# Optimization experiments

Measured on AMD Instinct MI355X. Metric: run time of the kernel, lower is better.

Reference implementation:

```python
import jax, jax.numpy as jnp
import numpy as np

EPS = 1e-5

def bn(x, g, b, mu, var):
    # inference-mode BatchNorm2d (InPlaceABNSync, activation='none')
    scale = g * jax.lax.rsqrt(var + EPS)
    shift = b - mu * scale
    return x * scale[None, :, None, None] + shift[None, :, None, None]

def conv1x1(x, w):
    # w: [C_out, C_in]; x: [B, C_in, H, W]
    return jnp.einsum('oc,bchw->bohw', w, x)

def block(x, w1, g1, b1, m1, v1, w2, g2, b2, m2, v2):
    # conv1x1 -> BN -> ReLU -> conv1x1 -> BN -> ReLU
    h = jax.nn.relu(bn(conv1x1(x, w1), g1, b1, m1, v1))
    return jax.nn.relu(bn(conv1x1(h, w2), g2, b2, m2, v2))

def setup_inputs() -> dict:
    key = jax.random.key(0)
    ks = jax.random.split(key, 24)
    B, HID, H, W = 8, 10, 512, 512
    MID = 32
    d = {}
    d['xf']  = jax.random.normal(ks[0], (B, HID, H, W), jnp.float32)
    d['xh1'] = jax.random.normal(ks[1], (B, HID, H, W), jnp.float32)
    d['xh2'] = jax.random.normal(ks[2], (B, HID, H, W), jnp.float32)
    def mk_bn(k, c):
        k1, k2, k3, k4 = jax.random.split(k, 4)
        return (jax.random.normal(k1, (c,), jnp.float32) * 0.1 + 1.0,
                jax.random.normal(k2, (c,), jnp.float32) * 0.1,
                jax.random.normal(k3, (c,), jnp.float32) * 0.1,
                jnp.abs(jax.random.normal(k4, (c,), jnp.float32)) * 0.5 + 0.5)
    # conv_hf params
    d['w_hf1'] = jax.random.normal(ks[3], (MID, 2 * HID), jnp.float32) * (1.0 / np.sqrt(2 * HID))
    d['g_hf1'], d['b_hf1'], d['m_hf1'], d['v_hf1'] = mk_bn(ks[4], MID)
    d['w_hf2'] = jax.random.normal(ks[5], (HID, MID), jnp.float32) * (1.0 / np.sqrt(MID))
    d['g_hf2'], d['b_hf2'], d['m_hf2'], d['v_hf2'] = mk_bn(ks[6], HID)
    # conv_update params
    d['w_up1'] = jax.random.normal(ks[7], (MID, 2 * HID), jnp.float32) * (1.0 / np.sqrt(2 * HID))
    d['g_up1'], d['b_up1'], d['m_up1'], d['v_up1'] = mk_bn(ks[8], MID)
    d['w_up2'] = jax.random.normal(ks[9], (HID, MID), jnp.float32) * (1.0 / np.sqrt(MID))
    d['g_up2'], d['b_up2'], d['m_up2'], d['v_up2'] = mk_bn(ks[10], HID)
    return d

def reference(xf, xh1, xh2,
              w_hf1, g_hf1, b_hf1, m_hf1, v_hf1,
              w_hf2, g_hf2, b_hf2, m_hf2, v_hf2,
              w_up1, g_up1, b_up1, m_up1, v_up1,
              w_up2, g_up2, b_up2, m_up2, v_up2):
    message = block(jnp.concatenate([xh1, xh2], axis=1),
                    w_hf1, g_hf1, b_hf1, m_hf1, v_hf1,
                    w_hf2, g_hf2, b_hf2, m_hf2, v_hf2)
    xf_new = block(jnp.concatenate([xf, message], axis=1),
                   w_up1, g_up1, b_up1, m_up1, v_up1,
                   w_up2, g_up2, b_up2, m_up2, v_up2)
    return (xf_new, message)
```

## Files before the change

kernel.cpp:

```cpp
#include <hip/hip_runtime.h>

#define EPS_BN 1e-5f
#define PLANE  262144u
#define IMG10  2621440u
#define MSGF   20971520u

typedef unsigned int u32;
typedef __fp16 h2 __attribute__((ext_vector_type(2)));
typedef _Float16 v8h __attribute__((ext_vector_type(8)));
typedef float v4f __attribute__((ext_vector_type(4)));

union W32 { u32 u; float f; h2 h; };
union AB  { u32 u[4]; uint4 q; v8h h; };

__device__ __forceinline__ u32 packh(float a, float b){
  W32 w; w.h.x = (__fp16)a; w.h.y = (__fp16)b; return w.u;
}

#if __has_builtin(__builtin_amdgcn_cvt_pkrtz)
__device__ __forceinline__ u32 pku(float a, float b){
  W32 w; w.h = __builtin_amdgcn_cvt_pkrtz(a, b); return w.u;
}
#else
__device__ __forceinline__ u32 pku(float a, float b){ return packh(a, b); }
#endif


__device__ __forceinline__ float wv(const float* w, int ncol, int row, int k){
  return (k >= 0) ? w[row*ncol + k] : 0.f;
}

extern "C" __global__ void prep_kernel(
  const float* __restrict__ w1, const float* __restrict__ g1, const float* __restrict__ b1, const float* __restrict__ m1, const float* __restrict__ v1,
  const float* __restrict__ w2, const float* __restrict__ g2, const float* __restrict__ b2, const float* __restrict__ m2, const float* __restrict__ v2,
  const float* __restrict__ w3, const float* __restrict__ g3, const float* __restrict__ b3, const float* __restrict__ m3, const float* __restrict__ v3,
  const float* __restrict__ w4, const float* __restrict__ g4, const float* __restrict__ b4, const float* __restrict__ m4, const float* __restrict__ v4,
  u32* __restrict__ ws)
{
  const int t = threadIdx.x;

  for (int r = 0; r < 2; r++){
    for (int i = t; i < 256; i += 256){
      int lane = i >> 2, tq = i & 3, g = lane >> 4, m = (lane & 15) + 16*r;
      int ka, kb;
      if      (tq == 0){ ka = g;                      kb = 4 + g; }
      else if (tq == 1){ ka = (g < 2) ? 8 + g : -1;   kb = 10 + g; }
      else if (tq == 2){ ka = 14 + g;                 kb = (g < 2) ? 18 + g : -1; }
      else             { ka = -1;                     kb = -1; }
      float sc = g1[m] * rsqrtf(v1[m] + EPS_BN);
      ws[256*r + i] = packh(wv(w1, 20, m, ka) * sc, wv(w1, 20, m, kb) * sc);
    }
  }
  for (int i = t; i < 256; i += 256){
    int lane = i >> 2, tq = i & 3, g = lane >> 4, m = lane & 15;
    int k0 = (tq < 2) ? (4*g + 2*tq) : (16 + 4*g + 2*(tq - 2));
    u32 val = 0u;
    if (m < 10){
      float sc = g2[m] * rsqrtf(v2[m] + EPS_BN);
      val = packh(w2[m*32 + k0] * sc, w2[m*32 + k0 + 1] * sc);
    }
    ws[512 + i] = val;
  }
  for (int r = 0; r < 2; r++){
    for (int i = t; i < 256; i += 256){
      int lane = i >> 2, tq = i & 3, g = lane >> 4, m = (lane & 15) + 16*r;
      int ka = -1, kb = -1;
      if (g == 0){ const int base[4] = {10, 12, 0, 2}; ka = base[tq]; kb = ka + 1; }
      else if (g == 1){ const int base[4] = {14, 16, 4, 6}; ka = base[tq]; kb = ka + 1; }
      else if (g == 2){ if (tq == 0){ ka = 18; kb = 19; } else if (tq == 1){ ka = 8; kb = 9; } }
      float sc = g3[m] * rsqrtf(v3[m] + EPS_BN);
      ws[768 + 256*r + i] = packh(wv(w3, 20, m, ka) * sc, wv(w3, 20, m, kb) * sc);
    }
  }
  for (int i = t; i < 256; i += 256){
    int lane = i >> 2, tq = i & 3, g = lane >> 4, m = lane & 15;
    int k0 = (tq < 2) ? (4*g + 2*tq) : (16 + 4*g + 2*(tq - 2));
    u32 val = 0u;
    if (m < 10){
      float sc = g4[m] * rsqrtf(v4[m] + EPS_BN);
      val = packh(w4[m*32 + k0] * sc, w4[m*32 + k0 + 1] * sc);
    }
    ws[1280 + i] = val;
  }
  for (int i = t; i < 32; i += 256){
    float sc = g1[i] * rsqrtf(v1[i] + EPS_BN);
    W32 w; w.f = b1[i] - m1[i] * sc; ws[1536 + i] = w.u;
  }
  for (int i = t; i < 16; i += 256){
    W32 w; w.f = 0.f;
    if (i < 10){ float sc = g2[i] * rsqrtf(v2[i] + EPS_BN); w.f = b2[i] - m2[i] * sc; }
    ws[1568 + i] = w.u;
  }
  for (int i = t; i < 32; i += 256){
    float sc = g3[i] * rsqrtf(v3[i] + EPS_BN);
    W32 w; w.f = b3[i] - m3[i] * sc; ws[1584 + i] = w.u;
  }
  for (int i = t; i < 16; i += 256){
    W32 w; w.f = 0.f;
    if (i < 10){ float sc = g4[i] * rsqrtf(v4[i] + EPS_BN); w.f = b4[i] - m4[i] * sc; }
    ws[1616 + i] = w.u;
  }
}

__device__ __forceinline__ v4f mfma16(const AB& a, const AB& b, v4f c){
  return __builtin_amdgcn_mfma_f32_16x16x32_f16(a.h, b.h, c, 0, 0, 0);
}

extern "C" __global__ __launch_bounds__(256) void fused_kernel(
  const float* __restrict__ xf, const float* __restrict__ xh1, const float* __restrict__ xh2,
  const u32* __restrict__ wsp, float* __restrict__ out)
{
  const unsigned tid  = threadIdx.x;
  const unsigned lane = tid & 63u;
  const unsigned c    = lane & 15u;
  const unsigned g    = lane >> 4;

  const uint4* W = (const uint4*)wsp;
  AB f1a, f1b, f2w, f3a, f3b, f4w;
  f1a.q = W[lane];        f1b.q = W[64 + lane];
  f2w.q = W[128 + lane];
  f3a.q = W[192 + lane];  f3b.q = W[256 + lane];
  f4w.q = W[320 + lane];
  const v4f* Bv = (const v4f*)(wsp + 1536);
  v4f c1a = Bv[g];
  v4f c1b = Bv[4 + g];
  v4f c2  = Bv[8 + g];
  v4f c3a = Bv[12 + g];
  v4f c3b = Bv[16 + g];
  v4f c4  = Bv[20 + g];

  const u32 soff0 = g * PLANE + c;
  const u32 soff1 = (4 + g) * PLANE + c;
  const u32 soff2 = (8 + g) * PLANE + c;
  const u32 xoff0 = (4*g + 0) * PLANE + c;
  const u32 xoff1 = (4*g + 1) * PLANE + c;
  const u32 xoff2 = (4*g + 2) * PLANE + c;
  const u32 xoff3 = (4*g + 3) * PLANE + c;
  const bool v8  = (g < 2);
  const bool vj0 = (4*g + 0 < 10), vj1 = (4*g + 1 < 10);
  const bool vj2 = (4*g + 2 < 10), vj3 = (4*g + 3 < 10);

  const unsigned wgl = blockIdx.x * 4u + (tid >> 6);

  #pragma unroll 2
  for (int it = 0; it < 16; ++it){
    const unsigned tile = wgl * 16u + it;
    const unsigned gp   = tile << 4;
    const unsigned b    = gp >> 18;
    const unsigned hw   = gp & (PLANE - 1u);
    const u32 pt = b * IMG10 + hw;

    float L0 = xh1[pt + soff0];
    float L1 = xh1[pt + soff1];
    float L2 = v8 ? xh1[pt + soff2] : 0.f;
    float L3 = xh2[pt + soff0];
    float L4 = xh2[pt + soff1];
    float L5 = v8 ? xh2[pt + soff2] : 0.f;
    float X0 = vj0 ? xf[pt + xoff0] : 0.f;
    float X1 = vj1 ? xf[pt + xoff1] : 0.f;
    float X2 = vj2 ? xf[pt + xoff2] : 0.f;
    float X3 = vj3 ? xf[pt + xoff3] : 0.f;

    AB b1u;
    b1u.u[0] = pku(L0, L1); b1u.u[1] = pku(L2, L3);
    b1u.u[2] = pku(L4, L5); b1u.u[3] = 0u;
    v4f d0 = mfma16(f1a, b1u, c1a);
    v4f d1 = mfma16(f1b, b1u, c1b);
    d0.x = fmaxf(d0.x, 0.f); d0.y = fmaxf(d0.y, 0.f); d0.z = fmaxf(d0.z, 0.f); d0.w = fmaxf(d0.w, 0.f);
    d1.x = fmaxf(d1.x, 0.f); d1.y = fmaxf(d1.y, 0.f); d1.z = fmaxf(d1.z, 0.f); d1.w = fmaxf(d1.w, 0.f);

    AB hb;
    hb.u[0] = pku(d0.x, d0.y); hb.u[1] = pku(d0.z, d0.w);
    hb.u[2] = pku(d1.x, d1.y); hb.u[3] = pku(d1.z, d1.w);
    v4f dm = mfma16(f2w, hb, c2);
    dm.x = fmaxf(dm.x, 0.f); dm.y = fmaxf(dm.y, 0.f); dm.z = fmaxf(dm.z, 0.f); dm.w = fmaxf(dm.w, 0.f);

    if (vj0) out[MSGF + pt + xoff0] = dm.x;
    if (vj1) out[MSGF + pt + xoff1] = dm.y;
    if (vj2) out[MSGF + pt + xoff2] = dm.z;
    if (vj3) out[MSGF + pt + xoff3] = dm.w;

    u32 mt0 = pku(dm.x, dm.y), mt1 = pku(dm.z, dm.w);
    u32 xt0 = pku(X0, X1),     xt1 = pku(X2, X3);
    AB b3u;
    b3u.u[0] = mt0;
    b3u.u[1] = (g == 2) ? xt0 : mt1;
    b3u.u[2] = xt0;
    b3u.u[3] = xt1;
    v4f e0 = mfma16(f3a, b3u, c3a);
    v4f e1 = mfma16(f3b, b3u, c3b);
    e0.x = fmaxf(e0.x, 0.f); e0.y = fmaxf(e0.y, 0.f); e0.z = fmaxf(e0.z, 0.f); e0.w = fmaxf(e0.w, 0.f);
    e1.x = fmaxf(e1.x, 0.f); e1.y = fmaxf(e1.y, 0.f); e1.z = fmaxf(e1.z, 0.f); e1.w = fmaxf(e1.w, 0.f);

    AB hb2;
    hb2.u[0] = pku(e0.x, e0.y); hb2.u[1] = pku(e0.z, e0.w);
    hb2.u[2] = pku(e1.x, e1.y); hb2.u[3] = pku(e1.z, e1.w);
    v4f dq = mfma16(f4w, hb2, c4);
    dq.x = fmaxf(dq.x, 0.f); dq.y = fmaxf(dq.y, 0.f); dq.z = fmaxf(dq.z, 0.f); dq.w = fmaxf(dq.w, 0.f);

    if (vj0) out[pt + xoff0] = dq.x;
    if (vj1) out[pt + xoff1] = dq.y;
    if (vj2) out[pt + xoff2] = dq.z;
    if (vj3) out[pt + xoff3] = dq.w;
  }
}

extern "C" void kernel_launch(void* const* d_in, const int* in_sizes, int n_in,
                              void* d_out, int out_size, void* d_ws, size_t ws_size,
                              hipStream_t stream)
{
  u32* ws = (u32*)d_ws;
  prep_kernel<<<1, 256, 0, stream>>>(
    (const float*)d_in[3],  (const float*)d_in[4],  (const float*)d_in[5],  (const float*)d_in[6],  (const float*)d_in[7],
    (const float*)d_in[8],  (const float*)d_in[9],  (const float*)d_in[10], (const float*)d_in[11], (const float*)d_in[12],
    (const float*)d_in[13], (const float*)d_in[14], (const float*)d_in[15], (const float*)d_in[16], (const float*)d_in[17],
    (const float*)d_in[18], (const float*)d_in[19], (const float*)d_in[20], (const float*)d_in[21], (const float*)d_in[22],
    ws);

  fused_kernel<<<2048, 256, 0, stream>>>(
    (const float*)d_in[0], (const float*)d_in[1], (const float*)d_in[2],
    ws, (float*)d_out);
}
```

Before: 426.8 us.

## Vectorize global loads and stores to float4 per lane with four MFMA columns

Each lane now loads and stores 16-byte float4 vectors covering four consecutive pixels instead of single floats. It runs the MFMA chain four times per tile, one per pixel slot, and transposes the results back into float4 stores. This cuts the number of memory instructions and widens each access to suit a bandwidth-bound kernel, at the cost of more live registers and fewer loop iterations to hide latency.

```diff
diff --git a/kernel.cpp b/kernel.cpp
--- a/kernel.cpp
+++ b/kernel.cpp
@@ -1,9 +1,9 @@
 #include <hip/hip_runtime.h>
 
 #define EPS_BN 1e-5f
-#define PLANE  262144u
-#define IMG10  2621440u
-#define MSGF   20971520u
+#define PLANE4  65536u
+#define IMG40   655360u
+#define MSGF4   5242880u
 
 typedef unsigned int u32;
 typedef __fp16 h2 __attribute__((ext_vector_type(2)));
@@ -106,9 +106,15 @@
   return __builtin_amdgcn_mfma_f32_16x16x32_f16(a.h, b.h, c, 0, 0, 0);
 }
 
+__device__ __forceinline__ v4f relu4(v4f v){
+  v.x = fmaxf(v.x, 0.f); v.y = fmaxf(v.y, 0.f);
+  v.z = fmaxf(v.z, 0.f); v.w = fmaxf(v.w, 0.f);
+  return v;
+}
+
 extern "C" __global__ __launch_bounds__(256) void fused_kernel(
-  const float* __restrict__ xf, const float* __restrict__ xh1, const float* __restrict__ xh2,
-  const u32* __restrict__ wsp, float* __restrict__ out)
+  const v4f* __restrict__ xf, const v4f* __restrict__ xh1, const v4f* __restrict__ xh2,
+  const u32* __restrict__ wsp, v4f* __restrict__ out)
 {
   const unsigned tid  = threadIdx.x;
   const unsigned lane = tid & 63u;
@@ -122,86 +128,97 @@
   f3a.q = W[192 + lane];  f3b.q = W[256 + lane];
   f4w.q = W[320 + lane];
   const v4f* Bv = (const v4f*)(wsp + 1536);
-  v4f c1a = Bv[g];
-  v4f c1b = Bv[4 + g];
+  v4f c1a = Bv[g];      v4f c1b = Bv[4 + g];
   v4f c2  = Bv[8 + g];
-  v4f c3a = Bv[12 + g];
-  v4f c3b = Bv[16 + g];
+  v4f c3a = Bv[12 + g]; v4f c3b = Bv[16 + g];
   v4f c4  = Bv[20 + g];
 
-  const u32 soff0 = g * PLANE + c;
-  const u32 soff1 = (4 + g) * PLANE + c;
-  const u32 soff2 = (8 + g) * PLANE + c;
-  const u32 xoff0 = (4*g + 0) * PLANE + c;
-  const u32 xoff1 = (4*g + 1) * PLANE + c;
-  const u32 xoff2 = (4*g + 2) * PLANE + c;
-  const u32 xoff3 = (4*g + 3) * PLANE + c;
-  const bool v8  = (g < 2);
-  const bool vj0 = (4*g + 0 < 10), vj1 = (4*g + 1 < 10);
-  const bool vj2 = (4*g + 2 < 10), vj3 = (4*g + 3 < 10);
+  const u32 po0 = g * PLANE4;
+  const u32 po1 = (4u + g) * PLANE4;
+  const u32 po2 = (8u + g) * PLANE4;
+  const u32 xo0 = (4u*g + 0u) * PLANE4;
+  const u32 xo1 = (4u*g + 1u) * PLANE4;
+  const u32 xo2 = (4u*g + 2u) * PLANE4;
+  const u32 xo3 = (4u*g + 3u) * PLANE4;
+  const bool v8  = (g < 2u);
+  const bool vj0 = (4u*g + 0u < 10u), vj1 = (4u*g + 1u < 10u);
+  const bool vj2 = (4u*g + 2u < 10u), vj3 = (4u*g + 3u < 10u);
 
   const unsigned wgl = blockIdx.x * 4u + (tid >> 6);
-
-  #pragma unroll 2
-  for (int it = 0; it < 16; ++it){
-    const unsigned tile = wgl * 16u + it;
-    const unsigned gp   = tile << 4;
-    const unsigned b    = gp >> 18;
-    const unsigned hw   = gp & (PLANE - 1u);
-    const u32 pt = b * IMG10 + hw;
-
-    float L0 = xh1[pt + soff0];
-    float L1 = xh1[pt + soff1];
-    float L2 = v8 ? xh1[pt + soff2] : 0.f;
-    float L3 = xh2[pt + soff0];
-    float L4 = xh2[pt + soff1];
-    float L5 = v8 ? xh2[pt + soff2] : 0.f;
-    float X0 = vj0 ? xf[pt + xoff0] : 0.f;
-    float X1 = vj1 ? xf[pt + xoff1] : 0.f;
-    float X2 = vj2 ? xf[pt + xoff2] : 0.f;
-    float X3 = vj3 ? xf[pt + xoff3] : 0.f;
-
-    AB b1u;
-    b1u.u[0] = pku(L0, L1); b1u.u[1] = pku(L2, L3);
-    b1u.u[2] = pku(L4, L5); b1u.u[3] = 0u;
-    v4f d0 = mfma16(f1a, b1u, c1a);
-    v4f d1 = mfma16(f1b, b1u, c1b);
-    d0.x = fmaxf(d0.x, 0.f); d0.y = fmaxf(d0.y, 0.f); d0.z = fmaxf(d0.z, 0.f); d0.w = fmaxf(d0.w, 0.f);
-    d1.x = fmaxf(d1.x, 0.f); d1.y = fmaxf(d1.y, 0.f); d1.z = fmaxf(d1.z, 0.f); d1.w = fmaxf(d1.w, 0.f);
-
-    AB hb;
-    hb.u[0] = pku(d0.x, d0.y); hb.u[1] = pku(d0.z, d0.w);
-    hb.u[2] = pku(d1.x, d1.y); hb.u[3] = pku(d1.z, d1.w);
-    v4f dm = mfma16(f2w, hb, c2);
-    dm.x = fmaxf(dm.x, 0.f); dm.y = fmaxf(dm.y, 0.f); dm.z = fmaxf(dm.z, 0.f); dm.w = fmaxf(dm.w, 0.f);
-
-    if (vj0) out[MSGF + pt + xoff0] = dm.x;
-    if (vj1) out[MSGF + pt + xoff1] = dm.y;
-    if (vj2) out[MSGF + pt + xoff2] = dm.z;
-    if (vj3) out[MSGF + pt + xoff3] = dm.w;
-
-    u32 mt0 = pku(dm.x, dm.y), mt1 = pku(dm.z, dm.w);
-    u32 xt0 = pku(X0, X1),     xt1 = pku(X2, X3);
-    AB b3u;
-    b3u.u[0] = mt0;
-    b3u.u[1] = (g == 2) ? xt0 : mt1;
-    b3u.u[2] = xt0;
-    b3u.u[3] = xt1;
-    v4f e0 = mfma16(f3a, b3u, c3a);
-    v4f e1 = mfma16(f3b, b3u, c3b);
-    e0.x = fmaxf(e0.x, 0.f); e0.y = fmaxf(e0.y, 0.f); e0.z = fmaxf(e0.z, 0.f); e0.w = fmaxf(e0.w, 0.f);
-    e1.x = fmaxf(e1.x, 0.f); e1.y = fmaxf(e1.y, 0.f); e1.z = fmaxf(e1.z, 0.f); e1.w = fmaxf(e1.w, 0.f);
-
-    AB hb2;
-    hb2.u[0] = pku(e0.x, e0.y); hb2.u[1] = pku(e0.z, e0.w);
-    hb2.u[2] = pku(e1.x, e1.y); hb2.u[3] = pku(e1.z, e1.w);
-    v4f dq = mfma16(f4w, hb2, c4);
-    dq.x = fmaxf(dq.x, 0.f); dq.y = fmaxf(dq.y, 0.f); dq.z = fmaxf(dq.z, 0.f); dq.w = fmaxf(dq.w, 0.f);
-
-    if (vj0) out[pt + xoff0] = dq.x;
-    if (vj1) out[pt + xoff1] = dq.y;
-    if (vj2) out[pt + xoff2] = dq.z;
-    if (vj3) out[pt + xoff3] = dq.w;
+  const v4f z4 = {0.f, 0.f, 0.f, 0.f};
+
+  for (int it = 0; it < 4; ++it){
+    const unsigned tile = wgl * 4u + (unsigned)it;
+    const unsigned q    = tile * 16u + c;
+    const unsigned b    = q >> 16;
+    const unsigned hw4  = q & (PLANE4 - 1u);
+    const u32 base4 = b * IMG40 + hw4;
+
+    v4f L0 = xh1[base4 + po0];
+    v4f L1 = xh1[base4 + po1];
+    v4f L2 = v8 ? xh1[base4 + po2] : z4;
+    v4f M0 = xh2[base4 + po0];
+    v4f M1 = xh2[base4 + po1];
+    v4f M2 = v8 ? xh2[base4 + po2] : z4;
+    v4f X0 = vj0 ? xf[base4 + xo0] : z4;
+    v4f X1 = vj1 ? xf[base4 + xo1] : z4;
+    v4f X2 = vj2 ? xf[base4 + xo2] : z4;
+    v4f X3 = vj3 ? xf[base4 + xo3] : z4;
+
+    u32 xt0[4], xt1[4];
+    #pragma unroll
+    for (int j = 0; j < 4; j++){ xt0[j] = pku(X0[j], X1[j]); xt1[j] = pku(X2[j], X3[j]); }
+
+    v4f dm[4];
+    #pragma unroll
+    for (int j = 0; j < 4; j++){
+      AB b1u;
+      b1u.u[0] = pku(L0[j], L1[j]);
+      b1u.u[1] = pku(L2[j], M0[j]);
+      b1u.u[2] = pku(M1[j], M2[j]);
+      b1u.u[3] = 0u;
+      v4f d0 = relu4(mfma16(f1a, b1u, c1a));
+      v4f d1 = relu4(mfma16(f1b, b1u, c1b));
+      AB hb;
+      hb.u[0] = pku(d0.x, d0.y); hb.u[1] = pku(d0.z, d0.w);
+      hb.u[2] = pku(d1.x, d1.y); hb.u[3] = pku(d1.z, d1.w);
+      dm[j] = relu4(mfma16(f2w, hb, c2));
+    }
+
+    if (vj0){ v4f r; r.x = dm[0].x; r.y = dm[1].x; r.z = dm[2].x; r.w = dm[3].x;
+              out[MSGF4 + base4 + xo0] = r; }
+    if (vj1){ v4f r; r.x = dm[0].y; r.y = dm[1].y; r.z = dm[2].y; r.w = dm[3].y;
+              out[MSGF4 + base4 + xo1] = r; }
+    if (vj2){ v4f r; r.x = dm[0].z; r.y = dm[1].z; r.z = dm[2].z; r.w = dm[3].z;
+              out[MSGF4 + base4 + xo2] = r; }
+    if (vj3){ v4f r; r.x = dm[0].w; r.y = dm[1].w; r.z = dm[2].w; r.w = dm[3].w;
+              out[MSGF4 + base4 + xo3] = r; }
+
+    v4f dq[4];
+    #pragma unroll
+    for (int j = 0; j < 4; j++){
+      u32 mt0 = pku(dm[j].x, dm[j].y), mt1 = pku(dm[j].z, dm[j].w);
+      AB b3u;
+      b3u.u[0] = mt0;
+      b3u.u[1] = (g == 2u) ? xt0[j] : mt1;
+      b3u.u[2] = xt0[j];
+      b3u.u[3] = xt1[j];
+      v4f e0 = relu4(mfma16(f3a, b3u, c3a));
+      v4f e1 = relu4(mfma16(f3b, b3u, c3b));
+      AB hb2;
+      hb2.u[0] = pku(e0.x, e0.y); hb2.u[1] = pku(e0.z, e0.w);
+      hb2.u[2] = pku(e1.x, e1.y); hb2.u[3] = pku(e1.z, e1.w);
+      dq[j] = relu4(mfma16(f4w, hb2, c4));
+    }
+
+    if (vj0){ v4f r; r.x = dq[0].x; r.y = dq[1].x; r.z = dq[2].x; r.w = dq[3].x;
+              out[base4 + xo0] = r; }
+    if (vj1){ v4f r; r.x = dq[0].y; r.y = dq[1].y; r.z = dq[2].y; r.w = dq[3].y;
+              out[base4 + xo1] = r; }
+    if (vj2){ v4f r; r.x = dq[0].z; r.y = dq[1].z; r.z = dq[2].z; r.w = dq[3].z;
+              out[base4 + xo2] = r; }
+    if (vj3){ v4f r; r.x = dq[0].w; r.y = dq[1].w; r.z = dq[2].w; r.w = dq[3].w;
+              out[base4 + xo3] = r; }
   }
 }
 
@@ -218,6 +235,6 @@
     ws);
 
   fused_kernel<<<2048, 256, 0, stream>>>(
-    (const float*)d_in[0], (const float*)d_in[1], (const float*)d_in[2],
-    ws, (float*)d_out);
-}
+    (const v4f*)d_in[0], (const v4f*)d_in[1], (const v4f*)d_in[2],
+    ws, (v4f*)d_out);
+}
```

New measurement: 387.8 us. 9.1% less time.
